# Kernel tuning notes

Hardware: AMD Instinct MI355X
Metric: run time of the kernel (lower is better)

Reference implementation:

```python
import jax, jax.numpy as jnp
import numpy as np

L, B, E, H = 1024, 8, 512, 8
D = E // H
THRESH = 0.1  # sparsity_threshold
W_STD = 0.1   # keeps logits spread so threshold mask is non-trivial


def setup_inputs() -> dict:
    k0 = jax.random.key(0)
    ks = jax.random.split(k0, 7)
    return {
        "query": jax.random.normal(ks[0], (L, B, E), jnp.float32),
        "key": jax.random.normal(ks[1], (L, B, E), jnp.float32),
        "value": jax.random.normal(ks[2], (L, B, E), jnp.float32),
        "Wq": jax.random.normal(ks[3], (E, E), jnp.float32) * W_STD,
        "bq": jnp.zeros((E,), jnp.float32),
        "Wk": jax.random.normal(ks[4], (E, E), jnp.float32) * W_STD,
        "bk": jnp.zeros((E,), jnp.float32),
    }


def reference(query, key, value, Wq, bq, Wk, bk):
    # query/key/value: (L, B, E), seq-first as in nn.MultiheadAttention
    Lq, Bq, Eq = query.shape
    S = key.shape[0]
    q = (query @ Wq.T + bq).reshape(Lq, Bq, H, D)
    k = (key @ Wk.T + bk).reshape(S, Bq, H, D)
    scale = 1.0 / jnp.sqrt(jnp.asarray(D, q.dtype))
    scores = jnp.einsum('lbhd,sbhd->bhls', q, k) * scale  # [B,H,L,S]
    attn = jax.nn.softmax(scores, axis=-1)
    attn_avg = attn.mean(axis=1)  # averaged over heads -> [B,L,S]
    # threshold-mask + renormalize
    sw = jnp.where(attn_avg > THRESH, attn_avg, jnp.zeros((), attn_avg.dtype))
    sw = sw / (sw.sum(axis=-1, keepdims=True) + 1e-6)
    # second matmul against the RAW value tensor: [B,L,S] @ [B,S,E] -> [L,B,E]
    out = jnp.einsum('bls,sbe->lbe', sw, value)
    return out, sw
```

## Files before the change

### kernel.cpp

```cpp
#include <hip/hip_runtime.h>


#define THRESH 0.1f
#define PLANE (8 * 8 * 1024 * 64)

typedef __attribute__((ext_vector_type(8))) short bf8_t;
typedef __attribute__((ext_vector_type(4))) float f4_t;

#define MFMA16(a, b, c) __builtin_amdgcn_mfma_f32_16x16x32_bf16(a, b, c, 0, 0, 0)

__device__ __forceinline__ unsigned short f2bf(float x) {
  unsigned int u = __float_as_uint(x);
  u += 0x7FFFu + ((u >> 16) & 1u);
  return (unsigned short)(u >> 16);
}
__device__ __forceinline__ float bf2f(unsigned short h) {
  return __uint_as_float(((unsigned int)h) << 16);
}

__global__ __launch_bounds__(256) void proj_kernel(
    const float* __restrict__ query, const float* __restrict__ key,
    const float* __restrict__ Wq,    const float* __restrict__ Wk,
    const float* __restrict__ bq,    const float* __restrict__ bk,
    unsigned short* __restrict__ outq, unsigned short* __restrict__ outk)
{
  const int z = blockIdx.z;
  const float* A    = z ? key : query;
  const float* W    = z ? Wk  : Wq;
  const float* bias = z ? bk  : bq;
  unsigned short* outp = z ? outk : outq;

  __shared__ float As[16][132];
  __shared__ float Ws[16][68];
  const int t  = threadIdx.x;
  const int bm = blockIdx.x;
  const int bn = blockIdx.y;
  const int ty = t >> 4;
  const int tx = t & 15;
  const int lr  = t >> 2;
  const int lc4 = (t & 3) << 2;

  const float* Arow0 = A + (size_t)(bm * 128 + lr) * 512 + lc4;
  const float* Arow1 = Arow0 + 64 * 512;
  const float* Wrow  = W + (size_t)(bn * 64 + lr) * 512 + lc4;

  float acc[8][4] = {};

  float4 a0 = *(const float4*)(Arow0);
  float4 a1 = *(const float4*)(Arow1);
  float4 w0 = *(const float4*)(Wrow);

  for (int k0 = 0; k0 < 512; k0 += 16) {
    __syncthreads();
    As[lc4 + 0][lr] = a0.x; As[lc4 + 1][lr] = a0.y; As[lc4 + 2][lr] = a0.z; As[lc4 + 3][lr] = a0.w;
    As[lc4 + 0][lr + 64] = a1.x; As[lc4 + 1][lr + 64] = a1.y; As[lc4 + 2][lr + 64] = a1.z; As[lc4 + 3][lr + 64] = a1.w;
    Ws[lc4 + 0][lr] = w0.x; Ws[lc4 + 1][lr] = w0.y; Ws[lc4 + 2][lr] = w0.z; Ws[lc4 + 3][lr] = w0.w;
    __syncthreads();
    if (k0 + 16 < 512) {
      a0 = *(const float4*)(Arow0 + k0 + 16);
      a1 = *(const float4*)(Arow1 + k0 + 16);
      w0 = *(const float4*)(Wrow  + k0 + 16);
    }
    #pragma unroll
    for (int kk = 0; kk < 16; ++kk) {
      float4 av0 = *(const float4*)&As[kk][ty * 8];
      float4 av1 = *(const float4*)&As[kk][ty * 8 + 4];
      float4 bv0 = *(const float4*)&Ws[kk][tx * 4];
      float ar[8] = {av0.x, av0.y, av0.z, av0.w, av1.x, av1.y, av1.z, av1.w};
      float br[4] = {bv0.x, bv0.y, bv0.z, bv0.w};
      #pragma unroll
      for (int i = 0; i < 8; ++i)
        #pragma unroll
        for (int j = 0; j < 4; ++j)
          acc[i][j] += ar[i] * br[j];
    }
  }

  const int h = bn;
  #pragma unroll
  for (int i = 0; i < 8; ++i) {
    const int gr = bm * 128 + ty * 8 + i;
    const int l = gr >> 3;
    const int b = gr & 7;
    const int d = tx * 4;
    const size_t off = ((size_t)((b * 8 + h) * 1024 + l)) * 64 + d;
    ushort4 ph, pm, pl;
    #pragma unroll
    for (int q = 0; q < 4; ++q) {
      float x = acc[i][q] + bias[h * 64 + d + q];
      unsigned short b1 = f2bf(x);  float r1 = x  - bf2f(b1);
      unsigned short b2 = f2bf(r1); float r2 = r1 - bf2f(b2);
      unsigned short b3 = f2bf(r2);
      ((unsigned short*)&ph)[q] = b1;
      ((unsigned short*)&pm)[q] = b2;
      ((unsigned short*)&pl)[q] = b3;
    }
    *(ushort4*)&outp[off] = ph;
    *(ushort4*)&outp[(size_t)PLANE + off] = pm;
    *(ushort4*)&outp[(size_t)2 * PLANE + off] = pl;
  }
}

__global__ __launch_bounds__(512, 1) void attn_mfma_kernel(
    const unsigned short* __restrict__ qs,
    const unsigned short* __restrict__ ks,
    float* __restrict__ sw)
{
  const int bx = blockIdx.x;
  const int b  = bx & 7;
  const int l0 = (bx >> 3) << 5;
  const int tid  = threadIdx.x;
  const int w    = tid >> 6;
  const int lane = tid & 63;
  const int c    = lane & 15;
  const int g    = lane >> 4;

  __shared__ float mred[2][8][32];
  __shared__ float sred[2][8][32];

#define KADDR(H, CT, KC, PL) \
  ((const bf8_t*)&ks[(size_t)(PL) * PLANE + \
      ((size_t)((b * 8 + (H)) * 1024 + w * 128 + (CT) * 16 + c)) * 64 + (KC) * 32 + g * 8])
#define QADDR(H, RT, KC, PL) \
  ((const bf8_t*)&qs[(size_t)(PL) * PLANE + \
      ((size_t)((b * 8 + (H)) * 1024 + l0 + (RT) * 16 + c)) * 64 + (KC) * 32 + g * 8])

  f4_t avg[2][8];
  #pragma unroll
  for (int rt = 0; rt < 2; ++rt)
    #pragma unroll
    for (int ct = 0; ct < 8; ++ct)
      avg[rt][ct] = (f4_t){0.f, 0.f, 0.f, 0.f};

  bf8_t kb[2][3];
  bf8_t qf[3][2][2];

  #pragma unroll
  for (int pl = 0; pl < 3; ++pl) {
    kb[0][pl] = *KADDR(0, 0, 0, pl);
    kb[1][pl] = *KADDR(0, 0, 1, pl);
    #pragma unroll
    for (int rt = 0; rt < 2; ++rt)
      #pragma unroll
      for (int kc = 0; kc < 2; ++kc)
        qf[pl][rt][kc] = *QADDR(0, rt, kc, pl);
  }

  for (int h = 0; h < 8; ++h) {
    const int par = h & 1;

    f4_t acc[2][8];
    #pragma unroll
    for (int rt = 0; rt < 2; ++rt)
      #pragma unroll
      for (int ct = 0; ct < 8; ++ct)
        acc[rt][ct] = (f4_t){0.f, 0.f, 0.f, 0.f};

    #pragma unroll
    for (int u = 0; u < 16; ++u) {
      const int ct = u >> 1, kc = u & 1, p = u & 1;
      const bf8_t kh = kb[p][0], km = kb[p][1], kl = kb[p][2];
      #pragma unroll
      for (int rt = 0; rt < 2; ++rt) {
        acc[rt][ct] = MFMA16(qf[0][rt][kc], kh, acc[rt][ct]);
        acc[rt][ct] = MFMA16(qf[0][rt][kc], km, acc[rt][ct]);
        acc[rt][ct] = MFMA16(qf[1][rt][kc], kh, acc[rt][ct]);
        acc[rt][ct] = MFMA16(qf[0][rt][kc], kl, acc[rt][ct]);
        acc[rt][ct] = MFMA16(qf[1][rt][kc], km, acc[rt][ct]);
        acc[rt][ct] = MFMA16(qf[2][rt][kc], kh, acc[rt][ct]);
      }
      if (u + 2 < 16) {
        #pragma unroll
        for (int pl = 0; pl < 3; ++pl)
          kb[p][pl] = *KADDR(h, (u + 2) >> 1, (u + 2) & 1, pl);
      } else if (h < 7) {
        #pragma unroll
        for (int pl = 0; pl < 3; ++pl)
          kb[p][pl] = *KADDR(h + 1, (u - 14) >> 1, u & 1, pl);
      }
    }

    if (h < 7) {
      #pragma unroll
      for (int pl = 0; pl < 3; ++pl)
        #pragma unroll
        for (int rt = 0; rt < 2; ++rt)
          #pragma unroll
          for (int kc = 0; kc < 2; ++kc)
            qf[pl][rt][kc] = *QADDR(h + 1, rt, kc, pl);
    }

    #pragma unroll
    for (int rt = 0; rt < 2; ++rt)
      #pragma unroll
      for (int reg = 0; reg < 4; ++reg) {
        float m = acc[rt][0][reg];
        #pragma unroll
        for (int ct = 1; ct < 8; ++ct) m = fmaxf(m, acc[rt][ct][reg]);
        #pragma unroll
        for (int off = 8; off > 0; off >>= 1) m = fmaxf(m, __shfl_xor(m, off));
        if (c == 0) mred[par][w][rt * 16 + g * 4 + reg] = m;
      }
    asm volatile("s_waitcnt lgkmcnt(0)\n\ts_barrier" ::: "memory");
    float mrow[2][4];
    #pragma unroll
    for (int rt = 0; rt < 2; ++rt) {
      float4 m4 = *(const float4*)&mred[par][0][rt * 16 + g * 4];
      #pragma unroll
      for (int w2 = 1; w2 < 8; ++w2) {
        float4 v = *(const float4*)&mred[par][w2][rt * 16 + g * 4];
        m4.x = fmaxf(m4.x, v.x); m4.y = fmaxf(m4.y, v.y);
        m4.z = fmaxf(m4.z, v.z); m4.w = fmaxf(m4.w, v.w);
      }
      mrow[rt][0] = m4.x; mrow[rt][1] = m4.y; mrow[rt][2] = m4.z; mrow[rt][3] = m4.w;
    }

    float sloc[2][4] = {};
    #pragma unroll
    for (int rt = 0; rt < 2; ++rt)
      #pragma unroll
      for (int ct = 0; ct < 8; ++ct)
        #pragma unroll
        for (int reg = 0; reg < 4; ++reg) {
          float p = __expf(0.125f * (acc[rt][ct][reg] - mrow[rt][reg]));
          acc[rt][ct][reg] = p;
          sloc[rt][reg] += p;
        }
    #pragma unroll
    for (int rt = 0; rt < 2; ++rt)
      #pragma unroll
      for (int reg = 0; reg < 4; ++reg) {
        float s = sloc[rt][reg];
        #pragma unroll
        for (int off = 8; off > 0; off >>= 1) s += __shfl_xor(s, off);
        if (c == 0) sred[par][w][rt * 16 + g * 4 + reg] = s;
      }
    asm volatile("s_waitcnt lgkmcnt(0)\n\ts_barrier" ::: "memory");
    #pragma unroll
    for (int rt = 0; rt < 2; ++rt) {
      float4 s4 = *(const float4*)&sred[par][0][rt * 16 + g * 4];
      #pragma unroll
      for (int w2 = 1; w2 < 8; ++w2) {
        float4 v = *(const float4*)&sred[par][w2][rt * 16 + g * 4];
        s4.x += v.x; s4.y += v.y; s4.z += v.z; s4.w += v.w;
      }
      float ssum[4] = {s4.x, s4.y, s4.z, s4.w};
      #pragma unroll
      for (int reg = 0; reg < 4; ++reg) {
        const float inv = 0.125f / ssum[reg];
        #pragma unroll
        for (int ct = 0; ct < 8; ++ct)
          avg[rt][ct][reg] += acc[rt][ct][reg] * inv;
      }
    }
  }

  float tl[2][4] = {};
  #pragma unroll
  for (int rt = 0; rt < 2; ++rt)
    #pragma unroll
    for (int ct = 0; ct < 8; ++ct)
      #pragma unroll
      for (int reg = 0; reg < 4; ++reg) {
        float v = avg[rt][ct][reg];
        v = v > THRESH ? v : 0.f;
        avg[rt][ct][reg] = v;
        tl[rt][reg] += v;
      }
  #pragma unroll
  for (int rt = 0; rt < 2; ++rt)
    #pragma unroll
    for (int reg = 0; reg < 4; ++reg) {
      float s = tl[rt][reg];
      #pragma unroll
      for (int off = 8; off > 0; off >>= 1) s += __shfl_xor(s, off);
      if (c == 0) mred[0][w][rt * 16 + g * 4 + reg] = s;
    }
  __syncthreads();
  #pragma unroll
  for (int rt = 0; rt < 2; ++rt) {
    float4 s4 = *(const float4*)&mred[0][0][rt * 16 + g * 4];
    #pragma unroll
    for (int w2 = 1; w2 < 8; ++w2) {
      float4 v = *(const float4*)&mred[0][w2][rt * 16 + g * 4];
      s4.x += v.x; s4.y += v.y; s4.z += v.z; s4.w += v.w;
    }
    float ts[4] = {s4.x, s4.y, s4.z, s4.w};
    #pragma unroll
    for (int reg = 0; reg < 4; ++reg) {
      const float inv = 1.f / (ts[reg] + 1e-6f);
      const size_t rowoff = ((size_t)(b * 1024 + l0 + rt * 16 + g * 4 + reg)) * 1024;
      #pragma unroll
      for (int ct = 0; ct < 8; ++ct)
        sw[rowoff + w * 128 + ct * 16 + c] = avg[rt][ct][reg] * inv;
    }
  }
#undef KADDR
#undef QADDR
}

__global__ __launch_bounds__(128) void pv_kernel(
    const float* __restrict__ sw,
    const float* __restrict__ value,
    float* __restrict__ out)
{
  const int l = blockIdx.x;
  const int b = blockIdx.y;
  const int t = threadIdx.x;
  __shared__ int cnt;
  __shared__ int   sidx[32];
  __shared__ float swt[32];
  if (t == 0) cnt = 0;
  __syncthreads();

  const float* row = sw + (size_t)(b * 1024 + l) * 1024;
  #pragma unroll
  for (int it = 0; it < 2; ++it) {
    const int s0 = (t + it * 128) * 4;
    float4 v = *(const float4*)(row + s0);
    if (v.x > 0.f) { int i = atomicAdd(&cnt, 1); if (i < 32) { sidx[i] = s0 + 0; swt[i] = v.x; } }
    if (v.y > 0.f) { int i = atomicAdd(&cnt, 1); if (i < 32) { sidx[i] = s0 + 1; swt[i] = v.y; } }
    if (v.z > 0.f) { int i = atomicAdd(&cnt, 1); if (i < 32) { sidx[i] = s0 + 2; swt[i] = v.z; } }
    if (v.w > 0.f) { int i = atomicAdd(&cnt, 1); if (i < 32) { sidx[i] = s0 + 3; swt[i] = v.w; } }
  }
  __syncthreads();
  const int n = cnt < 32 ? cnt : 32;

  const int e0 = t * 4;
  float4 o = {0.f, 0.f, 0.f, 0.f};
  for (int j = 0; j < n; ++j) {
    const float wgt = swt[j];
    const float4 vv = *(const float4*)(value + (size_t)(sidx[j] * 8 + b) * 512 + e0);
    o.x += wgt * vv.x; o.y += wgt * vv.y; o.z += wgt * vv.z; o.w += wgt * vv.w;
  }
  *(float4*)&out[(size_t)(l * 8 + b) * 512 + e0] = o;
}

extern "C" void kernel_launch(void* const* d_in, const int* in_sizes, int n_in,
                              void* d_out, int out_size, void* d_ws, size_t ws_size,
                              hipStream_t stream) {
  const float* query = (const float*)d_in[0];
  const float* key   = (const float*)d_in[1];
  const float* value = (const float*)d_in[2];
  const float* Wq    = (const float*)d_in[3];
  const float* bq    = (const float*)d_in[4];
  const float* Wk    = (const float*)d_in[5];
  const float* bk    = (const float*)d_in[6];

  float* out = (float*)d_out;
  float* sw  = out + (size_t)1024 * 8 * 512;

  unsigned short* qs = (unsigned short*)d_ws;
  unsigned short* ks = qs + (size_t)3 * PLANE;

  proj_kernel<<<dim3(64, 8, 2), 256, 0, stream>>>(query, key, Wq, Wk, bq, bk, qs, ks);
  attn_mfma_kernel<<<256, 512, 0, stream>>>(qs, ks, sw);
  pv_kernel<<<dim3(1024, 8), 128, 0, stream>>>(sw, value, out);
}
```

Baseline: 381.7 us.

## Stage K and Q tiles through swizzled LDS with double-buffered prefetch

The attention-score kernel now loads K and Q tiles cooperatively into LDS, using an XOR-swizzled layout and a double buffer for K, instead of having each wave read its fragments straight from global memory. The mapping of waves to key columns changes, so each 128-column tile is shared across the 8 waves and is written out in a different interleaved order. The aim is coalesced global loads and overlap of the next tile's fetch with MFMA work. In exchange it adds a block-wide __syncthreads per tile and more barriers in the softmax reductions, and uses about 120KB of LDS.

```diff
diff --git a/kernel.cpp b/kernel.cpp
--- a/kernel.cpp
+++ b/kernel.cpp
@@ -115,115 +115,171 @@
   const int c    = lane & 15;
   const int g    = lane >> 4;
 
-  __shared__ float mred[2][8][32];
-  __shared__ float sred[2][8][32];
-
-#define KADDR(H, CT, KC, PL) \
-  ((const bf8_t*)&ks[(size_t)(PL) * PLANE + \
-      ((size_t)((b * 8 + (H)) * 1024 + w * 128 + (CT) * 16 + c)) * 64 + (KC) * 32 + g * 8])
-#define QADDR(H, RT, KC, PL) \
-  ((const bf8_t*)&qs[(size_t)(PL) * PLANE + \
-      ((size_t)((b * 8 + (H)) * 1024 + l0 + (RT) * 16 + c)) * 64 + (KC) * 32 + g * 8])
+  __shared__ unsigned short Kl[2][3][128 * 64];
+  __shared__ unsigned short Ql[3][32 * 64];
+  __shared__ float red[8][32];
+
+  int kgo[6]; int klo[6];
+  #pragma unroll
+  for (int i = 0; i < 6; ++i) {
+    const int pos  = i * 8192 + tid * 16;
+    const int pl   = pos >> 14;
+    const int rem  = pos & 16383;
+    const int row  = rem >> 7;
+    const int slot = (rem >> 4) & 7;
+    const int src  = slot ^ (row & 7);
+    kgo[i] = pl * PLANE + (b * 8192 + row) * 64 + src * 8;
+    klo[i] = pl * 8192 + row * 64 + slot * 8;
+  }
+  int qgo[2]; int qlo[2];
+  #pragma unroll
+  for (int i = 0; i < 2; ++i) {
+    const int pos  = i * 8192 + tid * 16;
+    const int pl   = pos >> 12;
+    const int rem  = pos & 4095;
+    const int row  = rem >> 7;
+    const int slot = (rem >> 4) & 7;
+    const int src  = slot ^ (row & 7);
+    qgo[i] = pl * PLANE + (b * 8192 + l0 + row) * 64 + src * 8;
+    qlo[i] = pl * 2048 + row * 64 + slot * 8;
+  }
+  unsigned short* Kflat0 = &Kl[0][0][0];
+  unsigned short* Kflat1 = &Kl[1][0][0];
+  unsigned short* Qflat  = &Ql[0][0];
+
+  {
+    uint4 st[6];
+    #pragma unroll
+    for (int i = 0; i < 6; ++i) st[i] = *(const uint4*)(ks + kgo[i]);
+    uint4 q0 = *(const uint4*)(qs + qgo[0]);
+    uint4 q1 = {0,0,0,0};
+    if (tid < 256) q1 = *(const uint4*)(qs + qgo[1]);
+    #pragma unroll
+    for (int i = 0; i < 6; ++i) *(uint4*)(Kflat0 + klo[i]) = st[i];
+    *(uint4*)(Qflat + qlo[0]) = q0;
+    if (tid < 256) *(uint4*)(Qflat + qlo[1]) = q1;
+    __syncthreads();
+  }
 
   f4_t avg[2][8];
   #pragma unroll
   for (int rt = 0; rt < 2; ++rt)
     #pragma unroll
-    for (int ct = 0; ct < 8; ++ct)
-      avg[rt][ct] = (f4_t){0.f, 0.f, 0.f, 0.f};
-
-  bf8_t kb[2][3];
-  bf8_t qf[3][2][2];
-
-  #pragma unroll
-  for (int pl = 0; pl < 3; ++pl) {
-    kb[0][pl] = *KADDR(0, 0, 0, pl);
-    kb[1][pl] = *KADDR(0, 0, 1, pl);
-    #pragma unroll
-    for (int rt = 0; rt < 2; ++rt)
-      #pragma unroll
-      for (int kc = 0; kc < 2; ++kc)
-        qf[pl][rt][kc] = *QADDR(0, rt, kc, pl);
-  }
+    for (int t = 0; t < 8; ++t)
+      avg[rt][t] = (f4_t){0.f, 0.f, 0.f, 0.f};
+
+  const int krow  = w * 16 + c;
+  const int kst0  = (0 * 4 + g) ^ (krow & 7);
+  const int kst1  = (1 * 4 + g) ^ (krow & 7);
+  const int koff0 = krow * 64 + kst0 * 8;
+  const int koff1 = krow * 64 + kst1 * 8;
 
   for (int h = 0; h < 8; ++h) {
-    const int par = h & 1;
-
+    bf8_t qf[3][2][2];
     f4_t acc[2][8];
     #pragma unroll
     for (int rt = 0; rt < 2; ++rt)
       #pragma unroll
-      for (int ct = 0; ct < 8; ++ct)
-        acc[rt][ct] = (f4_t){0.f, 0.f, 0.f, 0.f};
-
-    #pragma unroll
-    for (int u = 0; u < 16; ++u) {
-      const int ct = u >> 1, kc = u & 1, p = u & 1;
-      const bf8_t kh = kb[p][0], km = kb[p][1], kl = kb[p][2];
-      #pragma unroll
-      for (int rt = 0; rt < 2; ++rt) {
-        acc[rt][ct] = MFMA16(qf[0][rt][kc], kh, acc[rt][ct]);
-        acc[rt][ct] = MFMA16(qf[0][rt][kc], km, acc[rt][ct]);
-        acc[rt][ct] = MFMA16(qf[1][rt][kc], kh, acc[rt][ct]);
-        acc[rt][ct] = MFMA16(qf[0][rt][kc], kl, acc[rt][ct]);
-        acc[rt][ct] = MFMA16(qf[1][rt][kc], km, acc[rt][ct]);
-        acc[rt][ct] = MFMA16(qf[2][rt][kc], kh, acc[rt][ct]);
-      }
-      if (u + 2 < 16) {
+      for (int t = 0; t < 8; ++t)
+        acc[rt][t] = (f4_t){0.f, 0.f, 0.f, 0.f};
+
+    #pragma unroll
+    for (int t = 0; t < 8; ++t) {
+      const int Tnext = h * 8 + t + 1;
+      const bool do_k = (Tnext < 64);
+      const bool do_q = (h < 7) && (t == 1);
+
+      uint4 st[6];
+      if (do_k) {
+        #pragma unroll
+        for (int i = 0; i < 6; ++i)
+          st[i] = *(const uint4*)(ks + kgo[i] + Tnext * 8192);
+      }
+      uint4 q0 = {0,0,0,0}, q1 = {0,0,0,0};
+      if (do_q) {
+        q0 = *(const uint4*)(qs + qgo[0] + (h + 1) * 65536);
+        if (tid < 256) q1 = *(const uint4*)(qs + qgo[1] + (h + 1) * 65536);
+      }
+
+      if (t == 0) {
         #pragma unroll
         for (int pl = 0; pl < 3; ++pl)
-          kb[p][pl] = *KADDR(h, (u + 2) >> 1, (u + 2) & 1, pl);
-      } else if (h < 7) {
-        #pragma unroll
-        for (int pl = 0; pl < 3; ++pl)
-          kb[p][pl] = *KADDR(h + 1, (u - 14) >> 1, u & 1, pl);
-      }
-    }
-
-    if (h < 7) {
-      #pragma unroll
-      for (int pl = 0; pl < 3; ++pl)
-        #pragma unroll
-        for (int rt = 0; rt < 2; ++rt)
           #pragma unroll
-          for (int kc = 0; kc < 2; ++kc)
-            qf[pl][rt][kc] = *QADDR(h + 1, rt, kc, pl);
-    }
-
+          for (int rt = 0; rt < 2; ++rt)
+            #pragma unroll
+            for (int kc = 0; kc < 2; ++kc) {
+              const int qrow = rt * 16 + c;
+              const int qstl = (kc * 4 + g) ^ (qrow & 7);
+              qf[pl][rt][kc] = *(const bf8_t*)(Qflat + pl * 2048 + qrow * 64 + qstl * 8);
+            }
+      }
+
+      {
+        const unsigned short* Kb = (t & 1) ? Kflat1 : Kflat0;
+        #pragma unroll
+        for (int kc = 0; kc < 2; ++kc) {
+          const int ko = kc ? koff1 : koff0;
+          bf8_t kf0 = *(const bf8_t*)(Kb + 0 * 8192 + ko);
+          bf8_t kf1 = *(const bf8_t*)(Kb + 1 * 8192 + ko);
+          bf8_t kf2 = *(const bf8_t*)(Kb + 2 * 8192 + ko);
+          #pragma unroll
+          for (int rt = 0; rt < 2; ++rt) {
+            acc[rt][t] = MFMA16(qf[0][rt][kc], kf0, acc[rt][t]);
+            acc[rt][t] = MFMA16(qf[0][rt][kc], kf1, acc[rt][t]);
+            acc[rt][t] = MFMA16(qf[1][rt][kc], kf0, acc[rt][t]);
+            acc[rt][t] = MFMA16(qf[0][rt][kc], kf2, acc[rt][t]);
+            acc[rt][t] = MFMA16(qf[1][rt][kc], kf1, acc[rt][t]);
+            acc[rt][t] = MFMA16(qf[2][rt][kc], kf0, acc[rt][t]);
+          }
+        }
+      }
+
+      if (do_k) {
+        unsigned short* Kd = (t & 1) ? Kflat0 : Kflat1;
+        #pragma unroll
+        for (int i = 0; i < 6; ++i) *(uint4*)(Kd + klo[i]) = st[i];
+      }
+      if (do_q) {
+        *(uint4*)(Qflat + qlo[0]) = q0;
+        if (tid < 256) *(uint4*)(Qflat + qlo[1]) = q1;
+      }
+      __syncthreads();
+    }
+
+    const int ridx = g * 4;
+    float mrow[2][4];
     #pragma unroll
     for (int rt = 0; rt < 2; ++rt)
       #pragma unroll
       for (int reg = 0; reg < 4; ++reg) {
         float m = acc[rt][0][reg];
         #pragma unroll
-        for (int ct = 1; ct < 8; ++ct) m = fmaxf(m, acc[rt][ct][reg]);
+        for (int t = 1; t < 8; ++t) m = fmaxf(m, acc[rt][t][reg]);
         #pragma unroll
         for (int off = 8; off > 0; off >>= 1) m = fmaxf(m, __shfl_xor(m, off));
-        if (c == 0) mred[par][w][rt * 16 + g * 4 + reg] = m;
-      }
-    asm volatile("s_waitcnt lgkmcnt(0)\n\ts_barrier" ::: "memory");
-    float mrow[2][4];
-    #pragma unroll
-    for (int rt = 0; rt < 2; ++rt) {
-      float4 m4 = *(const float4*)&mred[par][0][rt * 16 + g * 4];
-      #pragma unroll
-      for (int w2 = 1; w2 < 8; ++w2) {
-        float4 v = *(const float4*)&mred[par][w2][rt * 16 + g * 4];
-        m4.x = fmaxf(m4.x, v.x); m4.y = fmaxf(m4.y, v.y);
-        m4.z = fmaxf(m4.z, v.z); m4.w = fmaxf(m4.w, v.w);
-      }
-      mrow[rt][0] = m4.x; mrow[rt][1] = m4.y; mrow[rt][2] = m4.z; mrow[rt][3] = m4.w;
-    }
+        if (c == 0) red[w][rt * 16 + ridx + reg] = m;
+      }
+    __syncthreads();
+    #pragma unroll
+    for (int rt = 0; rt < 2; ++rt)
+      #pragma unroll
+      for (int reg = 0; reg < 4; ++reg) {
+        float m = red[0][rt * 16 + ridx + reg];
+        #pragma unroll
+        for (int w2 = 1; w2 < 8; ++w2) m = fmaxf(m, red[w2][rt * 16 + ridx + reg]);
+        mrow[rt][reg] = m;
+      }
+    __syncthreads();
 
     float sloc[2][4] = {};
     #pragma unroll
     for (int rt = 0; rt < 2; ++rt)
       #pragma unroll
-      for (int ct = 0; ct < 8; ++ct)
+      for (int t = 0; t < 8; ++t)
         #pragma unroll
         for (int reg = 0; reg < 4; ++reg) {
-          float p = __expf(0.125f * (acc[rt][ct][reg] - mrow[rt][reg]));
-          acc[rt][ct][reg] = p;
+          float p = __expf(0.125f * (acc[rt][t][reg] - mrow[rt][reg]));
+          acc[rt][t][reg] = p;
           sloc[rt][reg] += p;
         }
     #pragma unroll
@@ -233,38 +289,35 @@
         float s = sloc[rt][reg];
         #pragma unroll
         for (int off = 8; off > 0; off >>= 1) s += __shfl_xor(s, off);
-        if (c == 0) sred[par][w][rt * 16 + g * 4 + reg] = s;
-      }
-    asm volatile("s_waitcnt lgkmcnt(0)\n\ts_barrier" ::: "memory");
-    #pragma unroll
-    for (int rt = 0; rt < 2; ++rt) {
-      float4 s4 = *(const float4*)&sred[par][0][rt * 16 + g * 4];
-      #pragma unroll
-      for (int w2 = 1; w2 < 8; ++w2) {
-        float4 v = *(const float4*)&sred[par][w2][rt * 16 + g * 4];
-        s4.x += v.x; s4.y += v.y; s4.z += v.z; s4.w += v.w;
-      }
-      float ssum[4] = {s4.x, s4.y, s4.z, s4.w};
+        if (c == 0) red[w][rt * 16 + ridx + reg] = s;
+      }
+    __syncthreads();
+    #pragma unroll
+    for (int rt = 0; rt < 2; ++rt)
       #pragma unroll
       for (int reg = 0; reg < 4; ++reg) {
-        const float inv = 0.125f / ssum[reg];
-        #pragma unroll
-        for (int ct = 0; ct < 8; ++ct)
-          avg[rt][ct][reg] += acc[rt][ct][reg] * inv;
-      }
-    }
-  }
-
+        float s = red[0][rt * 16 + ridx + reg];
+        #pragma unroll
+        for (int w2 = 1; w2 < 8; ++w2) s += red[w2][rt * 16 + ridx + reg];
+        const float inv = 0.125f / s;
+        #pragma unroll
+        for (int t = 0; t < 8; ++t)
+          avg[rt][t][reg] += acc[rt][t][reg] * inv;
+      }
+    __syncthreads();
+  }
+
+  const int ridx = g * 4;
   float tl[2][4] = {};
   #pragma unroll
   for (int rt = 0; rt < 2; ++rt)
     #pragma unroll
-    for (int ct = 0; ct < 8; ++ct)
+    for (int t = 0; t < 8; ++t)
       #pragma unroll
       for (int reg = 0; reg < 4; ++reg) {
-        float v = avg[rt][ct][reg];
+        float v = avg[rt][t][reg];
         v = v > THRESH ? v : 0.f;
-        avg[rt][ct][reg] = v;
+        avg[rt][t][reg] = v;
         tl[rt][reg] += v;
       }
   #pragma unroll
@@ -274,29 +327,22 @@
       float s = tl[rt][reg];
       #pragma unroll
       for (int off = 8; off > 0; off >>= 1) s += __shfl_xor(s, off);
-      if (c == 0) mred[0][w][rt * 16 + g * 4 + reg] = s;
+      if (c == 0) red[w][rt * 16 + ridx + reg] = s;
     }
   __syncthreads();
   #pragma unroll
-  for (int rt = 0; rt < 2; ++rt) {
-    float4 s4 = *(const float4*)&mred[0][0][rt * 16 + g * 4];
-    #pragma unroll
-    for (int w2 = 1; w2 < 8; ++w2) {
-      float4 v = *(const float4*)&mred[0][w2][rt * 16 + g * 4];
-      s4.x += v.x; s4.y += v.y; s4.z += v.z; s4.w += v.w;
-    }
-    float ts[4] = {s4.x, s4.y, s4.z, s4.w};
+  for (int rt = 0; rt < 2; ++rt)
     #pragma unroll
     for (int reg = 0; reg < 4; ++reg) {
-      const float inv = 1.f / (ts[reg] + 1e-6f);
-      const size_t rowoff = ((size_t)(b * 1024 + l0 + rt * 16 + g * 4 + reg)) * 1024;
-      #pragma unroll
-      for (int ct = 0; ct < 8; ++ct)
-        sw[rowoff + w * 128 + ct * 16 + c] = avg[rt][ct][reg] * inv;
-    }
-  }
-#undef KADDR
-#undef QADDR
+      float s = red[0][rt * 16 + ridx + reg];
+      #pragma unroll
+      for (int w2 = 1; w2 < 8; ++w2) s += red[w2][rt * 16 + ridx + reg];
+      const float inv = 1.f / (s + 1e-6f);
+      const size_t rowoff = ((size_t)(b * 1024 + l0 + rt * 16 + ridx + reg)) * 1024;
+      #pragma unroll
+      for (int t = 0; t < 8; ++t)
+        sw[rowoff + t * 128 + w * 16 + c] = avg[rt][t][reg] * inv;
+    }
 }
 
 __global__ __launch_bounds__(128) void pv_kernel(
```

After: 414.0 us. 1.08x slower.
